# Kernel optimization log

Measured on AMD Instinct MI355X. Metric: run time of the kernel, lower is better.

The kernel has to match this reference:

```python
import jax, jax.numpy as jnp
import numpy as np

H = 64  # hidden_size
B, S, DIN = 256, 4096, 1
NUM_LAYERS = 3


def setup_inputs() -> dict:
    key = jax.random.key(0)
    ks = jax.random.split(key, 32)
    s = 1.0 / np.sqrt(H)  # torch LSTM/Linear init bound
    inp = {"x": jax.random.normal(ks[0], (B, S, DIN), dtype=jnp.float32)}
    ki = 1
    for l in range(NUM_LAYERS):
        din = DIN if l == 0 else H
        inp[f"Wih{l}"] = jax.random.uniform(ks[ki], (4 * H, din), minval=-s, maxval=s); ki += 1
        inp[f"Whh{l}"] = jax.random.uniform(ks[ki], (4 * H, H), minval=-s, maxval=s); ki += 1
        inp[f"bih{l}"] = jax.random.uniform(ks[ki], (4 * H,), minval=-s, maxval=s); ki += 1
        inp[f"bhh{l}"] = jax.random.uniform(ks[ki], (4 * H,), minval=-s, maxval=s); ki += 1
    inp["Wlin"] = jax.random.uniform(ks[ki], (1, H), minval=-s, maxval=s); ki += 1
    inp["blin"] = jax.random.uniform(ks[ki], (1,), minval=-s, maxval=s)
    return inp


def _lstm_layer(x, Wih, Whh, bih, bhh):
    """x: [B,S,Din] -> (hs [B,S,H], h_T [B,H], c_T [B,H]). PyTorch gate order i,f,g,o."""
    # precompute input contribution for all timesteps (one big GEMM)
    xg = jnp.einsum('bsd,gd->bsg', x, Wih) + (bih + bhh)  # [B,S,4H]
    b = x.shape[0]
    h0 = jnp.zeros((b, H), x.dtype)
    c0 = jnp.zeros((b, H), x.dtype)

    def step(carry, xg_t):
        h, c = carry
        g = xg_t + h @ Whh.T  # [B,4H]
        i, f, gg, o = jnp.split(g, 4, axis=-1)
        c = jax.nn.sigmoid(f) * c + jax.nn.sigmoid(i) * jnp.tanh(gg)
        h = jax.nn.sigmoid(o) * jnp.tanh(c)
        return (h, c), h

    (hT, cT), hs = jax.lax.scan(step, (h0, c0), jnp.swapaxes(xg, 0, 1))
    return jnp.swapaxes(hs, 0, 1), hT, cT


def reference(x, Wih0, Whh0, bih0, bhh0, Wih1, Whh1, bih1, bhh1,
              Wih2, Whh2, bih2, bhh2, Wlin, blin):
    layers = [(Wih0, Whh0, bih0, bhh0), (Wih1, Whh1, bih1, bhh1), (Wih2, Whh2, bih2, bhh2)]
    out = x
    hTs, cTs = [], []
    for (Wih, Whh, bih, bhh) in layers:
        out, hT, cT = _lstm_layer(out, Wih, Whh, bih, bhh)
        hTs.append(hT); cTs.append(cT)
    y = out @ Wlin.T + blin  # [B,S,1]
    h_n = jnp.stack(hTs, axis=0)  # [num_layers,B,H]
    c_n = jnp.stack(cTs, axis=0)
    return y, h_n, c_n
```

## Files before the change

kernel.cpp:

```cpp
#include <hip/hip_runtime.h>
#include <stdint.h>


#define SQ 4096
#define HH 64
#define NB 256

typedef _Float16 h2    __attribute__((ext_vector_type(2)));
typedef _Float16 f16x8 __attribute__((ext_vector_type(8)));
typedef float    f32x4 __attribute__((ext_vector_type(4)));

__device__ __forceinline__ float frcp(float x)  { return __builtin_amdgcn_rcpf(x); }
__device__ __forceinline__ float fexp2(float x) { return __builtin_amdgcn_exp2f(x); }

__device__ __forceinline__ void pin4(uint4& r) {
    asm volatile("" : "+v"(r.x), "+v"(r.y), "+v"(r.z), "+v"(r.w));
}
__device__ __forceinline__ void pinv(f32x4& r) {
    float t0 = r[0], t1 = r[1], t2 = r[2], t3 = r[3];
    asm volatile("" : "+v"(t0), "+v"(t1), "+v"(t2), "+v"(t3));
    r[0] = t0; r[1] = t1; r[2] = t2; r[3] = t3;
}

__device__ __forceinline__ f32x4 mm(uint4 hv, uint4 wv, f32x4 c) {
    return __builtin_amdgcn_mfma_f32_16x16x32_f16(
        __builtin_bit_cast(f16x8, hv), __builtin_bit_cast(f16x8, wv), c, 0, 0, 0);
}

__global__ __launch_bounds__(256)
void prep_weights(const float* __restrict__ Whh0, const float* __restrict__ Wih1,
                  const float* __restrict__ Whh1, const float* __restrict__ Wih2,
                  const float* __restrict__ Whh2, const float* __restrict__ Wlin,
                  uint32_t* __restrict__ ws)
{
    const int idx = blockIdx.x * 256 + threadIdx.x;
    if (idx >= 40960) {
        const int r  = idx - 40960;
        const int jj = r & 3;
        const int l  = (r >> 2) & 63;
        const int kk = (r >> 8) & 1;
        const int n  = l & 15;
        const int krow = ((l >> 4) << 3) + 2 * jj;
        const int ku   = 32 * kk + krow;
        h2 t;
        t[0] = (_Float16)((n == 0) ? Wlin[ku]     : 0.f);
        t[1] = (_Float16)((n == 0) ? Wlin[ku + 1] : 0.f);
        ws[idx] = __builtin_bit_cast(uint32_t, t);
        return;
    }
    int r, ktbits;
    const float *Wi = nullptr, *Wh;
    if (idx < 8192)       { r = idx;         ktbits = 1; Wh = Whh0; }
    else if (idx < 24576) { r = idx - 8192;  ktbits = 2; Wi = Wih1; Wh = Whh1; }
    else                  { r = idx - 24576; ktbits = 2; Wi = Wih2; Wh = Whh2; }
    const int jj  = r & 3;
    const int l   = (r >> 2) & 63;
    const int rem = r >> 8;
    const int kt  = rem & ((1 << ktbits) - 1);
    const int tw  = rem >> ktbits;
    const int j   = tw & 3;
    const int w   = tw >> 2;
    const int n   = l & 15;
    const int krow = ((l >> 4) << 3) + 2 * jj;
    const int orow = 64 * j + 16 * w + n;
    int kcol = 32 * kt + krow;
    const float* M;
    if (ktbits == 1)    { M = Wh; }
    else if (kcol < 64) { M = Wi; }
    else                { M = Wh; kcol -= 64; }
    h2 t;
    t[0] = (_Float16)M[orow * HH + kcol];
    t[1] = (_Float16)M[orow * HH + kcol + 1];
    ws[idx] = __builtin_bit_cast(uint32_t, t);
}

__global__ __launch_bounds__(768)
__attribute__((amdgpu_waves_per_eu(1, 3)))
void lstm3_fused(
    const float* __restrict__ x,
    const float* __restrict__ Wih0,
    const float* __restrict__ bih0, const float* __restrict__ bhh0,
    const float* __restrict__ bih1, const float* __restrict__ bhh1,
    const float* __restrict__ bih2, const float* __restrict__ bhh2,
    const float* __restrict__ blin,
    const uint32_t* __restrict__ wpk,
    float* __restrict__ out)
{
    const int b    = blockIdx.x;
    const int tid  = threadIdx.x;
    const int grp  = tid >> 8;
    const int k    = tid & 255;
    const int w    = k >> 6;
    const int l    = k & 63;
    const int n    = l & 15;
    const int q    = l >> 4;
    const int unit = 16 * w + n;
    const bool grp0w1 = (grp == 0) && (w == 1);

    __shared__ __align__(16) float xrow[SQ + 4];
    __shared__ __align__(16) uint4 hbf[2][3][8];
    __shared__ __align__(16) float ystage[32];

    for (int i = tid; i < SQ; i += 768) xrow[i] = x[b * SQ + i];
    if (tid < 4) xrow[SQ + tid] = 0.f;
    if (tid < 48) ((uint4*)hbf)[tid] = make_uint4(0, 0, 0, 0);

    const int gbase = (grp == 0) ? 0 : (grp == 1) ? 8192 : 24576;
    const int KT    = (grp == 0) ? 2 : 4;
    const uint32_t* wbp = wpk + gbase;
    auto fr = [&](int j_, int kt_) {
        return *reinterpret_cast<const uint4*>(
            wbp + (((w * 4 + j_) * KT + kt_) * 64 + l) * 4);
    };
    uint4 w00 = fr(0, 0), w01 = fr(0, 1), w10 = fr(1, 0), w11 = fr(1, 1),
          w20 = fr(2, 0), w21 = fr(2, 1), w30 = fr(3, 0), w31 = fr(3, 1);
    pin4(w00); pin4(w01); pin4(w10); pin4(w11);
    pin4(w20); pin4(w21); pin4(w30); pin4(w31);
    uint4 w02 = {}, w03 = {}, w12 = {}, w13 = {},
          w22 = {}, w23 = {}, w32 = {}, w33 = {};
    if (grp != 0) {
        w02 = fr(0, 2); w03 = fr(0, 3); w12 = fr(1, 2); w13 = fr(1, 3);
        w22 = fr(2, 2); w23 = fr(2, 3); w32 = fr(3, 2); w33 = fr(3, 3);
        pin4(w02); pin4(w03); pin4(w12); pin4(w13);
        pin4(w22); pin4(w23); pin4(w32); pin4(w33);
    }
    uint4 wy2 = {}, wy3 = {};
    f32x4 cy = {0.f, 0.f, 0.f, 0.f};
    if (grp0w1) {
        wy2 = *reinterpret_cast<const uint4*>(wpk + 40960 + (0 * 64 + l) * 4);
        wy3 = *reinterpret_cast<const uint4*>(wpk + 40960 + (1 * 64 + l) * 4);
        pin4(wy2); pin4(wy3);
        const float bv = blin[0];
        cy = f32x4{bv, bv, bv, bv};
        pinv(cy);
    }

    const float* bi = (grp == 0) ? bih0 : (grp == 1) ? bih1 : bih2;
    const float* bh = (grp == 0) ? bhh0 : (grp == 1) ? bhh1 : bhh2;
    const float bs0 = bi[unit]       + bh[unit];
    const float bs1 = bi[64 + unit]  + bh[64 + unit];
    const float bs2 = bi[128 + unit] + bh[128 + unit];
    const float bs3 = bi[192 + unit] + bh[192 + unit];
    f32x4 cb0 = {bs0, bs0, bs0, bs0};  pinv(cb0);
    f32x4 cb1 = {bs1, bs1, bs1, bs1};  pinv(cb1);
    f32x4 cb2 = {bs2, bs2, bs2, bs2};  pinv(cb2);
    f32x4 cb3 = {bs3, bs3, bs3, bs3};  pinv(cb3);

    float wx0 = 0.f, wx1 = 0.f, wx2 = 0.f, wx3 = 0.f;
    if (grp == 0) {
        wx0 = Wih0[unit];       wx1 = Wih0[64 + unit];
        wx2 = Wih0[128 + unit]; wx3 = Wih0[192 + unit];
    }

    const int la = (grp == 2) ? 1 : 0;
    const int lb = grp;
    const uint4* pA[2] = { &hbf[0][la][q], &hbf[1][la][q] };
    const uint4* pB[2] = { &hbf[0][lb][q], &hbf[1][lb][q] };
    const uint4* pY[2] = { &hbf[0][2][q],  &hbf[1][2][q] };
    _Float16* pH[2] = { (_Float16*)&hbf[0][grp][0] + unit,
                        (_Float16*)&hbf[1][grp][0] + unit };

    float cc = 0.f;

    __syncthreads();

    auto tick = [&](int T, int rd) {
        const int wr = rd ^ 1;
        float xT = 0.f;
        if (grp == 0) xT = xrow[T];

        const uint4 a0 = pA[rd][0], a1 = pA[rd][4];
        f32x4 d0 = mm(a0, w00, cb0);
        f32x4 d1 = mm(a0, w10, cb1);
        f32x4 d2 = mm(a0, w20, cb2);
        f32x4 d3 = mm(a0, w30, cb3);
        d0 = mm(a1, w01, d0);  d1 = mm(a1, w11, d1);
        d2 = mm(a1, w21, d2);  d3 = mm(a1, w31, d3);
        if (grp != 0) {
            const uint4 c0 = pB[rd][0], c1 = pB[rd][4];
            d0 = mm(c0, w02, d0);  d1 = mm(c0, w12, d1);
            d2 = mm(c0, w22, d2);  d3 = mm(c0, w32, d3);
            d0 = mm(c1, w03, d0);  d1 = mm(c1, w13, d1);
            d2 = mm(c1, w23, d2);  d3 = mm(c1, w33, d3);
        }

        if (grp0w1) {
            const int sy = T - 3;
            if (sy >= 0 && sy < SQ) {
                const uint4 y0 = pY[rd][0], y1 = pY[rd][4];
                f32x4 d4 = mm(y0, wy2, cy);
                d4 = mm(y1, wy3, d4);
                if (l == 0) ystage[sy & 31] = d4[0];
                if ((sy & 31) == 31) {
                    const float yv = ystage[l & 31];
                    if (l < 32) out[b * SQ + (sy - 31) + l] = yv;
                }
            }
        }

        const int step = T - grp;
        if (step >= 0 && step < SQ) {
            float gi = d0[0], gf = d1[0], gg = d2[0], go = d3[0];
            if (grp == 0) {
                gi += wx0 * xT; gf += wx1 * xT;
                gg += wx2 * xT; go += wx3 * xT;
            }
            const float i_ = frcp(1.f + fexp2(gi * -1.44269504f));
            const float f_ = frcp(1.f + fexp2(gf * -1.44269504f));
            const float o_ = frcp(1.f + fexp2(go * -1.44269504f));
            const float tg = 2.f * frcp(1.f + fexp2(gg * -2.88539008f)) - 1.f;
            cc = f_ * cc + i_ * tg;
            const float tc = fminf(fmaxf(cc, -15.f), 15.f);
            const float e  = fexp2(tc * -2.88539008f);
            const float h  = o_ * ((1.f - e) * frcp(1.f + e));
            if (l < 16) {
                pH[wr][0] = (_Float16)h;
                if (step == SQ - 1) {
                    out[NB * SQ + grp * NB * HH + b * HH + unit] = h;
                    out[NB * SQ + 3 * NB * HH + grp * NB * HH + b * HH + unit] = cc;
                }
            }
        }
        __syncthreads();
    };

    for (int T = 0; T < SQ + 4; T += 2) {
        tick(T, 0);
        tick(T + 1, 1);
    }
}

extern "C" void kernel_launch(void* const* d_in, const int* in_sizes, int n_in,
                              void* d_out, int out_size, void* d_ws, size_t ws_size,
                              hipStream_t stream) {
    const float* x    = (const float*)d_in[0];
    const float* Wih0 = (const float*)d_in[1];
    const float* Whh0 = (const float*)d_in[2];
    const float* bih0 = (const float*)d_in[3];
    const float* bhh0 = (const float*)d_in[4];
    const float* Wih1 = (const float*)d_in[5];
    const float* Whh1 = (const float*)d_in[6];
    const float* bih1 = (const float*)d_in[7];
    const float* bhh1 = (const float*)d_in[8];
    const float* Wih2 = (const float*)d_in[9];
    const float* Whh2 = (const float*)d_in[10];
    const float* bih2 = (const float*)d_in[11];
    const float* bhh2 = (const float*)d_in[12];
    const float* Wlin = (const float*)d_in[13];
    const float* blin = (const float*)d_in[14];
    float* out = (float*)d_out;

    uint32_t* wpk = (uint32_t*)d_ws;
    prep_weights<<<162, 256, 0, stream>>>(Whh0, Wih1, Whh1, Wih2, Whh2, Wlin, wpk);
    lstm3_fused<<<NB, 768, 0, stream>>>(x, Wih0, bih0, bhh0,
                                        bih1, bhh1, bih2, bhh2,
                                        blin, wpk, out);
}
```

Before: 2.580 ms.

## Replace block-wide barriers with per-wave LDS flag spin-waits and dedicated head wave

Drops the __syncthreads per timestep and instead has each wave publish a progress counter in shared memory. Consumers spin on the min of their producer, self-group and consumer flags, using a 4-deep ring buffer of hidden states so layers can drift apart by up to a few steps. The linear output head moves to its own 13th wave so the layer waves do less work per step. This is meant to cut barrier latency on the serial recurrence, at the cost of spin polling traffic on LDS, a bounded spin that could silently give up after a fixed iteration count, and reliance on relaxed atomics plus waitcnt for ordering.

```diff
diff --git a/kernel.cpp b/kernel.cpp
--- a/kernel.cpp
+++ b/kernel.cpp
@@ -20,6 +20,13 @@
     float t0 = r[0], t1 = r[1], t2 = r[2], t3 = r[3];
     asm volatile("" : "+v"(t0), "+v"(t1), "+v"(t2), "+v"(t3));
     r[0] = t0; r[1] = t1; r[2] = t2; r[3] = t3;
+}
+
+__device__ __forceinline__ uint32_t fld(const uint32_t* p) {
+    return __hip_atomic_load(p, __ATOMIC_RELAXED, __HIP_MEMORY_SCOPE_WORKGROUP);
+}
+__device__ __forceinline__ void fst(uint32_t* p, uint32_t v) {
+    __hip_atomic_store(p, v, __ATOMIC_RELAXED, __HIP_MEMORY_SCOPE_WORKGROUP);
 }
 
 __device__ __forceinline__ f32x4 mm(uint4 hv, uint4 wv, f32x4 c) {
@@ -74,8 +81,8 @@
     ws[idx] = __builtin_bit_cast(uint32_t, t);
 }
 
-__global__ __launch_bounds__(768)
-__attribute__((amdgpu_waves_per_eu(1, 3)))
+__global__ __launch_bounds__(832)
+__attribute__((amdgpu_waves_per_eu(1, 4)))
 void lstm3_fused(
     const float* __restrict__ x,
     const float* __restrict__ Wih0,
@@ -88,88 +95,122 @@
 {
     const int b    = blockIdx.x;
     const int tid  = threadIdx.x;
-    const int grp  = tid >> 8;
-    const int k    = tid & 255;
-    const int w    = k >> 6;
-    const int l    = k & 63;
+    const int wid  = tid >> 6;
+    const int l    = tid & 63;
     const int n    = l & 15;
     const int q    = l >> 4;
+    const bool is_head = (wid == 12);
+    const int grp  = wid >> 2;
+    const int w    = wid & 3;
     const int unit = 16 * w + n;
-    const bool grp0w1 = (grp == 0) && (w == 1);
-
-    __shared__ __align__(16) float xrow[SQ + 4];
-    __shared__ __align__(16) uint4 hbf[2][3][8];
+
+    __shared__ __align__(16) float xrow[SQ];
+    __shared__ __align__(16) uint4 hb[4][3][8];
     __shared__ __align__(16) float ystage[32];
-
-    for (int i = tid; i < SQ; i += 768) xrow[i] = x[b * SQ + i];
-    if (tid < 4) xrow[SQ + tid] = 0.f;
-    if (tid < 48) ((uint4*)hbf)[tid] = make_uint4(0, 0, 0, 0);
-
-    const int gbase = (grp == 0) ? 0 : (grp == 1) ? 8192 : 24576;
-    const int KT    = (grp == 0) ? 2 : 4;
-    const uint32_t* wbp = wpk + gbase;
-    auto fr = [&](int j_, int kt_) {
-        return *reinterpret_cast<const uint4*>(
-            wbp + (((w * 4 + j_) * KT + kt_) * 64 + l) * 4);
+    __shared__ uint32_t pflags[16];
+
+    for (int i = tid; i < SQ; i += 832) xrow[i] = x[b * SQ + i];
+    if (tid < 96) ((uint4*)hb)[tid] = make_uint4(0, 0, 0, 0);
+    if (tid < 16) pflags[tid] = (tid > 12) ? 0x7fffffffu : 0u;
+
+    auto min4 = [&](int base) -> int {
+        uint32_t a  = fld(&pflags[base]);
+        uint32_t b1 = fld(&pflags[base + 1]);
+        uint32_t c  = fld(&pflags[base + 2]);
+        uint32_t d  = fld(&pflags[base + 3]);
+        uint32_t m0 = a < b1 ? a : b1;
+        uint32_t m1 = c < d ? c : d;
+        return (int)(m0 < m1 ? m0 : m1);
     };
-    uint4 w00 = fr(0, 0), w01 = fr(0, 1), w10 = fr(1, 0), w11 = fr(1, 1),
-          w20 = fr(2, 0), w21 = fr(2, 1), w30 = fr(3, 0), w31 = fr(3, 1);
-    pin4(w00); pin4(w01); pin4(w10); pin4(w11);
-    pin4(w20); pin4(w21); pin4(w30); pin4(w31);
-    uint4 w02 = {}, w03 = {}, w12 = {}, w13 = {},
-          w22 = {}, w23 = {}, w32 = {}, w33 = {};
-    if (grp != 0) {
-        w02 = fr(0, 2); w03 = fr(0, 3); w12 = fr(1, 2); w13 = fr(1, 3);
-        w22 = fr(2, 2); w23 = fr(2, 3); w32 = fr(3, 2); w33 = fr(3, 3);
-        pin4(w02); pin4(w03); pin4(w12); pin4(w13);
-        pin4(w22); pin4(w23); pin4(w32); pin4(w33);
-    }
+
+    uint4 w00 = {}, w01 = {}, w10 = {}, w11 = {}, w20 = {}, w21 = {}, w30 = {}, w31 = {};
+    uint4 w02 = {}, w03 = {}, w12 = {}, w13 = {}, w22 = {}, w23 = {}, w32 = {}, w33 = {};
     uint4 wy2 = {}, wy3 = {};
-    f32x4 cy = {0.f, 0.f, 0.f, 0.f};
-    if (grp0w1) {
+    f32x4 cb0 = {}, cb1 = {}, cb2 = {}, cb3 = {}, cy = {};
+    float wx0 = 0.f, wx1 = 0.f, wx2 = 0.f, wx3 = 0.f;
+
+    if (is_head) {
         wy2 = *reinterpret_cast<const uint4*>(wpk + 40960 + (0 * 64 + l) * 4);
         wy3 = *reinterpret_cast<const uint4*>(wpk + 40960 + (1 * 64 + l) * 4);
         pin4(wy2); pin4(wy3);
         const float bv = blin[0];
         cy = f32x4{bv, bv, bv, bv};
         pinv(cy);
-    }
-
-    const float* bi = (grp == 0) ? bih0 : (grp == 1) ? bih1 : bih2;
-    const float* bh = (grp == 0) ? bhh0 : (grp == 1) ? bhh1 : bhh2;
-    const float bs0 = bi[unit]       + bh[unit];
-    const float bs1 = bi[64 + unit]  + bh[64 + unit];
-    const float bs2 = bi[128 + unit] + bh[128 + unit];
-    const float bs3 = bi[192 + unit] + bh[192 + unit];
-    f32x4 cb0 = {bs0, bs0, bs0, bs0};  pinv(cb0);
-    f32x4 cb1 = {bs1, bs1, bs1, bs1};  pinv(cb1);
-    f32x4 cb2 = {bs2, bs2, bs2, bs2};  pinv(cb2);
-    f32x4 cb3 = {bs3, bs3, bs3, bs3};  pinv(cb3);
-
-    float wx0 = 0.f, wx1 = 0.f, wx2 = 0.f, wx3 = 0.f;
-    if (grp == 0) {
-        wx0 = Wih0[unit];       wx1 = Wih0[64 + unit];
-        wx2 = Wih0[128 + unit]; wx3 = Wih0[192 + unit];
-    }
-
-    const int la = (grp == 2) ? 1 : 0;
-    const int lb = grp;
-    const uint4* pA[2] = { &hbf[0][la][q], &hbf[1][la][q] };
-    const uint4* pB[2] = { &hbf[0][lb][q], &hbf[1][lb][q] };
-    const uint4* pY[2] = { &hbf[0][2][q],  &hbf[1][2][q] };
-    _Float16* pH[2] = { (_Float16*)&hbf[0][grp][0] + unit,
-                        (_Float16*)&hbf[1][grp][0] + unit };
-
+    } else {
+        const int gbase = (grp == 0) ? 0 : (grp == 1) ? 8192 : 24576;
+        const int KT    = (grp == 0) ? 2 : 4;
+        const uint32_t* wbp = wpk + gbase;
+        auto fr = [&](int j_, int kt_) {
+            return *reinterpret_cast<const uint4*>(
+                wbp + (((w * 4 + j_) * KT + kt_) * 64 + l) * 4);
+        };
+        w00 = fr(0, 0); w01 = fr(0, 1); w10 = fr(1, 0); w11 = fr(1, 1);
+        w20 = fr(2, 0); w21 = fr(2, 1); w30 = fr(3, 0); w31 = fr(3, 1);
+        pin4(w00); pin4(w01); pin4(w10); pin4(w11);
+        pin4(w20); pin4(w21); pin4(w30); pin4(w31);
+        if (grp != 0) {
+            w02 = fr(0, 2); w03 = fr(0, 3); w12 = fr(1, 2); w13 = fr(1, 3);
+            w22 = fr(2, 2); w23 = fr(2, 3); w32 = fr(3, 2); w33 = fr(3, 3);
+            pin4(w02); pin4(w03); pin4(w12); pin4(w13);
+            pin4(w22); pin4(w23); pin4(w32); pin4(w33);
+        }
+        const float* bi = (grp == 0) ? bih0 : (grp == 1) ? bih1 : bih2;
+        const float* bh = (grp == 0) ? bhh0 : (grp == 1) ? bhh1 : bhh2;
+        const float bs0 = bi[unit]       + bh[unit];
+        const float bs1 = bi[64 + unit]  + bh[64 + unit];
+        const float bs2 = bi[128 + unit] + bh[128 + unit];
+        const float bs3 = bi[192 + unit] + bh[192 + unit];
+        cb0 = f32x4{bs0, bs0, bs0, bs0};  pinv(cb0);
+        cb1 = f32x4{bs1, bs1, bs1, bs1};  pinv(cb1);
+        cb2 = f32x4{bs2, bs2, bs2, bs2};  pinv(cb2);
+        cb3 = f32x4{bs3, bs3, bs3, bs3};  pinv(cb3);
+        if (grp == 0) {
+            wx0 = Wih0[unit];       wx1 = Wih0[64 + unit];
+            wx2 = Wih0[128 + unit]; wx3 = Wih0[192 + unit];
+        }
+    }
+
+    __syncthreads();
+
+    if (is_head) {
+        for (int s = 0; s < SQ; ++s) {
+            for (int gu = 0; gu < 131072; ++gu) {
+                if (min4(8) >= s + 1) break;
+            }
+            asm volatile("s_waitcnt lgkmcnt(0)" ::: "memory");
+            const uint4* py = &hb[s & 3][2][q];
+            const uint4 y0 = py[0], y1 = py[4];
+            f32x4 d4 = mm(y0, wy2, cy);
+            d4 = mm(y1, wy3, d4);
+            if (l == 0) ystage[s & 31] = d4[0];
+            asm volatile("s_waitcnt lgkmcnt(0)" ::: "memory");
+            if (l == 0) fst(&pflags[12], (uint32_t)(s + 1));
+            if ((s & 31) == 31) {
+                const float yv = ystage[l & 31];
+                if (l < 32) out[b * SQ + (s - 31) + l] = yv;
+            }
+        }
+        return;
+    }
+
+    const int la    = (grp == 2) ? 1 : 0;
+    const int selfb = grp * 4;
+    const int prodb = (grp - 1) * 4;
+    const int consb = (grp + 1) * 4;
     float cc = 0.f;
 
-    __syncthreads();
-
-    auto tick = [&](int T, int rd) {
-        const int wr = rd ^ 1;
-        float xT = 0.f;
-        if (grp == 0) xT = xrow[T];
-
-        const uint4 a0 = pA[rd][0], a1 = pA[rd][4];
+    for (int s = 0; s < SQ; ++s) {
+        for (int gu = 0; gu < 131072; ++gu) {
+            bool ok = (min4(selfb) >= s);
+            if (grp != 0) ok = ok && (min4(prodb) >= s + 1);
+            ok = ok && (min4(consb) >= s - 3);
+            if (ok) break;
+        }
+        asm volatile("s_waitcnt lgkmcnt(0)" ::: "memory");
+
+        const int sa = s & 3, sb = (s + 3) & 3;
+        const uint4* pa = &hb[(grp == 0) ? sb : sa][la][q];
+        const uint4 a0 = pa[0], a1 = pa[4];
         f32x4 d0 = mm(a0, w00, cb0);
         f32x4 d1 = mm(a0, w10, cb1);
         f32x4 d2 = mm(a0, w20, cb2);
@@ -177,56 +218,37 @@
         d0 = mm(a1, w01, d0);  d1 = mm(a1, w11, d1);
         d2 = mm(a1, w21, d2);  d3 = mm(a1, w31, d3);
         if (grp != 0) {
-            const uint4 c0 = pB[rd][0], c1 = pB[rd][4];
+            const uint4* pbp = &hb[sb][grp][q];
+            const uint4 c0 = pbp[0], c1 = pbp[4];
             d0 = mm(c0, w02, d0);  d1 = mm(c0, w12, d1);
             d2 = mm(c0, w22, d2);  d3 = mm(c0, w32, d3);
             d0 = mm(c1, w03, d0);  d1 = mm(c1, w13, d1);
             d2 = mm(c1, w23, d2);  d3 = mm(c1, w33, d3);
         }
 
-        if (grp0w1) {
-            const int sy = T - 3;
-            if (sy >= 0 && sy < SQ) {
-                const uint4 y0 = pY[rd][0], y1 = pY[rd][4];
-                f32x4 d4 = mm(y0, wy2, cy);
-                d4 = mm(y1, wy3, d4);
-                if (l == 0) ystage[sy & 31] = d4[0];
-                if ((sy & 31) == 31) {
-                    const float yv = ystage[l & 31];
-                    if (l < 32) out[b * SQ + (sy - 31) + l] = yv;
-                }
+        float gi = d0[0], gf = d1[0], gg = d2[0], go = d3[0];
+        if (grp == 0) {
+            const float xT = xrow[s];
+            gi += wx0 * xT; gf += wx1 * xT;
+            gg += wx2 * xT; go += wx3 * xT;
+        }
+        const float i_ = frcp(1.f + fexp2(gi * -1.44269504f));
+        const float f_ = frcp(1.f + fexp2(gf * -1.44269504f));
+        const float o_ = frcp(1.f + fexp2(go * -1.44269504f));
+        const float tg = 2.f * frcp(1.f + fexp2(gg * -2.88539008f)) - 1.f;
+        cc = f_ * cc + i_ * tg;
+        const float tc = fminf(fmaxf(cc, -15.f), 15.f);
+        const float e  = fexp2(tc * -2.88539008f);
+        const float h  = o_ * ((1.f - e) * frcp(1.f + e));
+        if (l < 16) {
+            *((_Float16*)&hb[sa][grp][0] + unit) = (_Float16)h;
+            if (s == SQ - 1) {
+                out[NB * SQ + grp * NB * HH + b * HH + unit] = h;
+                out[NB * SQ + 3 * NB * HH + grp * NB * HH + b * HH + unit] = cc;
             }
         }
-
-        const int step = T - grp;
-        if (step >= 0 && step < SQ) {
-            float gi = d0[0], gf = d1[0], gg = d2[0], go = d3[0];
-            if (grp == 0) {
-                gi += wx0 * xT; gf += wx1 * xT;
-                gg += wx2 * xT; go += wx3 * xT;
-            }
-            const float i_ = frcp(1.f + fexp2(gi * -1.44269504f));
-            const float f_ = frcp(1.f + fexp2(gf * -1.44269504f));
-            const float o_ = frcp(1.f + fexp2(go * -1.44269504f));
-            const float tg = 2.f * frcp(1.f + fexp2(gg * -2.88539008f)) - 1.f;
-            cc = f_ * cc + i_ * tg;
-            const float tc = fminf(fmaxf(cc, -15.f), 15.f);
-            const float e  = fexp2(tc * -2.88539008f);
-            const float h  = o_ * ((1.f - e) * frcp(1.f + e));
-            if (l < 16) {
-                pH[wr][0] = (_Float16)h;
-                if (step == SQ - 1) {
-                    out[NB * SQ + grp * NB * HH + b * HH + unit] = h;
-                    out[NB * SQ + 3 * NB * HH + grp * NB * HH + b * HH + unit] = cc;
-                }
-            }
-        }
-        __syncthreads();
-    };
-
-    for (int T = 0; T < SQ + 4; T += 2) {
-        tick(T, 0);
-        tick(T + 1, 1);
+        asm volatile("s_waitcnt lgkmcnt(0)" ::: "memory");
+        if (l == 0) fst(&pflags[selfb + w], (uint32_t)(s + 1));
     }
 }
 
@@ -252,7 +274,7 @@
 
     uint32_t* wpk = (uint32_t*)d_ws;
     prep_weights<<<162, 256, 0, stream>>>(Whh0, Wih1, Whh1, Wih2, Whh2, Wlin, wpk);
-    lstm3_fused<<<NB, 768, 0, stream>>>(x, Wih0, bih0, bhh0,
+    lstm3_fused<<<NB, 832, 0, stream>>>(x, Wih0, bih0, bhh0,
                                         bih1, bhh1, bih2, bhh2,
                                         blin, wpk, out);
 }
```

Measured after the change: 3.687 ms. 1.43x slower.

## Skew layers via ring buffers and batch input projections every 16 steps

Applied to the files above, without the earlier changes.

Replaces the lockstep one-step-per-layer wavefront with a skewed schedule in which layers 1 and 2 run a fixed number of steps behind the layer below. Hidden states are kept in 32-entry shared-memory ring buffers. Every 16 steps, each upper layer computes the input-to-hidden projection for the next 16 timesteps in one batch of MFMAs (using the 16 N columns as timesteps) and stores it in shared memory. This takes the input projection off the per-step critical path, leaving only the recurrent matmul per step. In exchange it adds shared-memory traffic and a longer pipeline fill/drain tail, and the skew and ring sizes must stay consistent to avoid reading stale or overwritten hidden states.

```diff
diff --git a/kernel.cpp b/kernel.cpp
--- a/kernel.cpp
+++ b/kernel.cpp
@@ -5,6 +5,9 @@
 #define SQ 4096
 #define HH 64
 #define NB 256
+#define SK1 18
+#define SK2 36
+#define SKH 38
 
 typedef _Float16 h2    __attribute__((ext_vector_type(2)));
 typedef _Float16 f16x8 __attribute__((ext_vector_type(8)));
@@ -96,14 +99,15 @@
     const int q    = l >> 4;
     const int unit = 16 * w + n;
     const bool grp0w1 = (grp == 0) && (w == 1);
-
-    __shared__ __align__(16) float xrow[SQ + 4];
-    __shared__ __align__(16) uint4 hbf[2][3][8];
+    const int wg   = (tid >> 6) - 4;
+
+    __shared__ __align__(16) float xrow[SQ];
+    __shared__ __align__(16) _Float16 ring[3][32][72];
+    __shared__ __align__(16) float gin[8][16][4][16];
     __shared__ __align__(16) float ystage[32];
 
     for (int i = tid; i < SQ; i += 768) xrow[i] = x[b * SQ + i];
-    if (tid < 4) xrow[SQ + tid] = 0.f;
-    if (tid < 48) ((uint4*)hbf)[tid] = make_uint4(0, 0, 0, 0);
+    for (int i = tid; i < 864; i += 768) ((uint4*)ring)[i] = make_uint4(0, 0, 0, 0);
 
     const int gbase = (grp == 0) ? 0 : (grp == 1) ? 8192 : 24576;
     const int KT    = (grp == 0) ? 2 : 4;
@@ -152,81 +156,113 @@
         wx2 = Wih0[128 + unit]; wx3 = Wih0[192 + unit];
     }
 
-    const int la = (grp == 2) ? 1 : 0;
-    const int lb = grp;
-    const uint4* pA[2] = { &hbf[0][la][q], &hbf[1][la][q] };
-    const uint4* pB[2] = { &hbf[0][lb][q], &hbf[1][lb][q] };
-    const uint4* pY[2] = { &hbf[0][2][q],  &hbf[1][2][q] };
-    _Float16* pH[2] = { (_Float16*)&hbf[0][grp][0] + unit,
-                        (_Float16*)&hbf[1][grp][0] + unit };
-
+    const f32x4 Z = {0.f, 0.f, 0.f, 0.f};
     float cc = 0.f;
+    const int skew = (grp == 1) ? SK1 : SK2;
 
     __syncthreads();
 
-    auto tick = [&](int T, int rd) {
-        const int wr = rd ^ 1;
-        float xT = 0.f;
-        if (grp == 0) xT = xrow[T];
-
-        const uint4 a0 = pA[rd][0], a1 = pA[rd][4];
-        f32x4 d0 = mm(a0, w00, cb0);
-        f32x4 d1 = mm(a0, w10, cb1);
-        f32x4 d2 = mm(a0, w20, cb2);
-        f32x4 d3 = mm(a0, w30, cb3);
-        d0 = mm(a1, w01, d0);  d1 = mm(a1, w11, d1);
-        d2 = mm(a1, w21, d2);  d3 = mm(a1, w31, d3);
-        if (grp != 0) {
-            const uint4 c0 = pB[rd][0], c1 = pB[rd][4];
-            d0 = mm(c0, w02, d0);  d1 = mm(c0, w12, d1);
-            d2 = mm(c0, w22, d2);  d3 = mm(c0, w32, d3);
-            d0 = mm(c1, w03, d0);  d1 = mm(c1, w13, d1);
-            d2 = mm(c1, w23, d2);  d3 = mm(c1, w33, d3);
-        }
-
-        if (grp0w1) {
-            const int sy = T - 3;
-            if (sy >= 0 && sy < SQ) {
-                const uint4 y0 = pY[rd][0], y1 = pY[rd][4];
-                f32x4 d4 = mm(y0, wy2, cy);
-                d4 = mm(y1, wy3, d4);
-                if (l == 0) ystage[sy & 31] = d4[0];
-                if ((sy & 31) == 31) {
-                    const float yv = ystage[l & 31];
-                    if (l < 32) out[b * SQ + (sy - 31) + l] = yv;
+    for (int T = 0; T < SQ + SKH; ++T) {
+        if (grp == 0) {
+            const _Float16* sp = &ring[0][(T + 31) & 31][0];
+            const uint4 a0 = *(const uint4*)(sp + q * 8);
+            const uint4 a1 = *(const uint4*)(sp + 32 + q * 8);
+            f32x4 d0 = mm(a0, w00, cb0); d0 = mm(a1, w01, d0);
+            f32x4 d1 = mm(a0, w10, cb1); d1 = mm(a1, w11, d1);
+            f32x4 d2 = mm(a0, w20, cb2); d2 = mm(a1, w21, d2);
+            f32x4 d3 = mm(a0, w30, cb3); d3 = mm(a1, w31, d3);
+
+            if (grp0w1) {
+                const int sy = T - SKH;
+                if (sy >= 0) {
+                    const _Float16* hp = &ring[2][sy & 31][0];
+                    const uint4 y0 = *(const uint4*)(hp + q * 8);
+                    const uint4 y1 = *(const uint4*)(hp + 32 + q * 8);
+                    f32x4 d4 = mm(y0, wy2, cy);
+                    d4 = mm(y1, wy3, d4);
+                    if (l == 0) ystage[sy & 31] = d4[0];
+                    if ((sy & 31) == 31) {
+                        const float yv = ystage[l & 31];
+                        if (l < 32) out[b * SQ + (sy - 31) + l] = yv;
+                    }
                 }
             }
-        }
-
-        const int step = T - grp;
-        if (step >= 0 && step < SQ) {
-            float gi = d0[0], gf = d1[0], gg = d2[0], go = d3[0];
-            if (grp == 0) {
-                gi += wx0 * xT; gf += wx1 * xT;
-                gg += wx2 * xT; go += wx3 * xT;
+
+            if (T < SQ) {
+                const float xT = xrow[T];
+                float gi = d0[0] + wx0 * xT;
+                float gf = d1[0] + wx1 * xT;
+                float gg = d2[0] + wx2 * xT;
+                float go = d3[0] + wx3 * xT;
+                const float i_ = frcp(1.f + fexp2(gi * -1.44269504f));
+                const float f_ = frcp(1.f + fexp2(gf * -1.44269504f));
+                const float o_ = frcp(1.f + fexp2(go * -1.44269504f));
+                const float tg = 2.f * frcp(1.f + fexp2(gg * -2.88539008f)) - 1.f;
+                cc = f_ * cc + i_ * tg;
+                const float tc = fminf(fmaxf(cc, -15.f), 15.f);
+                const float e  = fexp2(tc * -2.88539008f);
+                const float h  = o_ * ((1.f - e) * frcp(1.f + e));
+                if (l < 16) {
+                    ring[0][T & 31][unit] = (_Float16)h;
+                    if (T == SQ - 1) {
+                        out[NB * SQ + b * HH + unit] = h;
+                        out[NB * SQ + 3 * NB * HH + b * HH + unit] = cc;
+                    }
+                }
             }
-            const float i_ = frcp(1.f + fexp2(gi * -1.44269504f));
-            const float f_ = frcp(1.f + fexp2(gf * -1.44269504f));
-            const float o_ = frcp(1.f + fexp2(go * -1.44269504f));
-            const float tg = 2.f * frcp(1.f + fexp2(gg * -2.88539008f)) - 1.f;
-            cc = f_ * cc + i_ * tg;
-            const float tc = fminf(fmaxf(cc, -15.f), 15.f);
-            const float e  = fexp2(tc * -2.88539008f);
-            const float h  = o_ * ((1.f - e) * frcp(1.f + e));
-            if (l < 16) {
-                pH[wr][0] = (_Float16)h;
-                if (step == SQ - 1) {
-                    out[NB * SQ + grp * NB * HH + b * HH + unit] = h;
-                    out[NB * SQ + 3 * NB * HH + grp * NB * HH + b * HH + unit] = cc;
+        } else {
+            const int s = T - skew;
+            if (s >= 0) {
+                if ((s & 15) == 0 && s < SQ) {
+                    const _Float16* bp = &ring[grp - 1][(s + n) & 31][q * 8];
+                    const uint4 ab0 = *(const uint4*)bp;
+                    const uint4 ab1 = *(const uint4*)(bp + 32);
+                    f32x4 e0 = mm(ab0, w00, Z); e0 = mm(ab1, w01, e0);
+                    f32x4 e1 = mm(ab0, w10, Z); e1 = mm(ab1, w11, e1);
+                    f32x4 e2 = mm(ab0, w20, Z); e2 = mm(ab1, w21, e2);
+                    f32x4 e3 = mm(ab0, w30, Z); e3 = mm(ab1, w31, e3);
+#pragma unroll
+                    for (int jj = 0; jj < 4; ++jj) {
+                        gin[wg][q * 4 + jj][0][n] = e0[jj];
+                        gin[wg][q * 4 + jj][1][n] = e1[jj];
+                        gin[wg][q * 4 + jj][2][n] = e2[jj];
+                        gin[wg][q * 4 + jj][3][n] = e3[jj];
+                    }
+                }
+
+                const _Float16* sp = &ring[grp][(s + 31) & 31][0];
+                const uint4 c0 = *(const uint4*)(sp + q * 8);
+                const uint4 c1 = *(const uint4*)(sp + 32 + q * 8);
+                f32x4 d0 = mm(c0, w02, cb0); d0 = mm(c1, w03, d0);
+                f32x4 d1 = mm(c0, w12, cb1); d1 = mm(c1, w13, d1);
+                f32x4 d2 = mm(c0, w22, cb2); d2 = mm(c1, w23, d2);
+                f32x4 d3 = mm(c0, w32, cb3); d3 = mm(c1, w33, d3);
+
+                if (s < SQ) {
+                    const int r = s & 15;
+                    float gi = d0[0] + gin[wg][r][0][n];
+                    float gf = d1[0] + gin[wg][r][1][n];
+                    float gg = d2[0] + gin[wg][r][2][n];
+                    float go = d3[0] + gin[wg][r][3][n];
+                    const float i_ = frcp(1.f + fexp2(gi * -1.44269504f));
+                    const float f_ = frcp(1.f + fexp2(gf * -1.44269504f));
+                    const float o_ = frcp(1.f + fexp2(go * -1.44269504f));
+                    const float tg = 2.f * frcp(1.f + fexp2(gg * -2.88539008f)) - 1.f;
+                    cc = f_ * cc + i_ * tg;
+                    const float tc = fminf(fmaxf(cc, -15.f), 15.f);
+                    const float e  = fexp2(tc * -2.88539008f);
+                    const float h  = o_ * ((1.f - e) * frcp(1.f + e));
+                    if (l < 16) {
+                        ring[grp][s & 31][unit] = (_Float16)h;
+                        if (s == SQ - 1) {
+                            out[NB * SQ + grp * NB * HH + b * HH + unit] = h;
+                            out[NB * SQ + 3 * NB * HH + grp * NB * HH + b * HH + unit] = cc;
+                        }
+                    }
                 }
             }
         }
         __syncthreads();
-    };
-
-    for (int T = 0; T < SQ + 4; T += 2) {
-        tick(T, 0);
-        tick(T + 1, 1);
     }
 }
 
```

New measurement: 2.325 ms. 9.9% less time.
